# Performance work log

Hardware: AMD Instinct MI355X
Metric: run time of the kernel (lower is better)

Reference implementation:

```python
import jax, jax.numpy as jnp
import numpy as np

B, T, CTX, D, L, H, FF, NMODES = 1024, 512, 23, 320, 5, 8, 1280, 48
DH = D // H
EPS = 1e-5


def layernorm(x, w, b):
    m = jnp.mean(x, axis=-1, keepdims=True)
    v = jnp.mean(jnp.square(x - m), axis=-1, keepdims=True)
    return (x - m) * jax.lax.rsqrt(v + EPS) * w + b


def cheb_sum(x, c):
    """sum_n c[:, n] * T_n(x) via the Chebyshev recurrence, fused with the
    reduction (Clenshaw-style accumulation, no (B,T,N+1) intermediate).
    x: (B,T) in [-1,1], c: (B, N+1)."""
    t_prev = jnp.ones_like(x)           # T_0
    t_cur = x                           # T_1
    acc = c[:, 0:1] * t_prev + c[:, 1:2] * t_cur

    def step(carry, cn):
        tp, tc, a = carry
        tn = 2.0 * x * tc - tp          # T_{n+1}
        return (tc, tn, a + cn[:, None] * tn), None

    (_, _, acc), _ = jax.lax.scan(step, (t_prev, t_cur, acc),
                                  jnp.swapaxes(c[:, 2:], 0, 1))
    return acc


def _forward(k_norm, ctx, W_e, b_e, cls, ln1_w, ln1_b, W_in, b_in, W_out, b_out,
             ln2_w, ln2_b, W1, b1, W2, b2, hln_w, hln_b, Wh1, bh1, Wh2, bh2):
    Bc = ctx.shape[0]
    # elem_proj: Linear(1, D) applied per scalar token -> (B, CTX, D)
    tok = ctx[..., None] * W_e + b_e
    x = jnp.concatenate([jnp.broadcast_to(cls, (Bc, 1, D)), tok], axis=1)  # (B, 24, D)

    def layer(x, p):
        l1w, l1b, win, bin_, wout, bout, l2w, l2b, w1, b1_, w2, b2_ = p
        # --- pre-norm self attention ---
        h = layernorm(x, l1w, l1b)
        qkv = h @ win.T + bin_                      # (B, S, 3D)
        q, k, v = jnp.split(qkv, 3, axis=-1)
        S = x.shape[1]
        q = q.reshape(Bc, S, H, DH)
        k = k.reshape(Bc, S, H, DH)
        v = v.reshape(Bc, S, H, DH)
        scores = jnp.einsum('bqhd,bkhd->bhqk', q, k) / np.sqrt(DH).astype(np.float32)
        a = jax.nn.softmax(scores, axis=-1)
        o = jnp.einsum('bhqk,bkhd->bqhd', a, v).reshape(Bc, S, D)
        x = x + o @ wout.T + bout
        # --- pre-norm FFN ---
        h2 = layernorm(x, l2w, l2b)
        x = x + jax.nn.gelu(h2 @ w1.T + b1_, approximate=False) @ w2.T + b2_
        return x, None

    x, _ = jax.lax.scan(layer, x, (ln1_w, ln1_b, W_in, b_in, W_out, b_out,
                                   ln2_w, ln2_b, W1, b1, W2, b2))
    h = layernorm(x[:, 0], hln_w, hln_b)            # CLS pooling + head LN
    c = jax.nn.gelu(h @ Wh1.T + bh1, approximate=False) @ Wh2.T + bh2  # (B, N+1)
    z = cheb_sum(k_norm, c)
    return jax.nn.sigmoid(z)


def setup_inputs() -> dict:
    key = jax.random.key(0)
    ks = jax.random.split(key, 24)
    rn = lambda k, sh, s=0.02: jax.random.normal(k, sh, jnp.float32) * s
    return {
        'k_norm': jax.random.uniform(ks[0], (B, T), jnp.float32, -1.0, 1.0),
        'ctx': jax.random.normal(ks[1], (B, CTX), jnp.float32),
        'W_e': rn(ks[2], (D,), 0.5),
        'b_e': jnp.zeros((D,), jnp.float32),
        'cls': rn(ks[3], (1, 1, D)),
        'ln1_w': jnp.ones((L, D), jnp.float32),
        'ln1_b': jnp.zeros((L, D), jnp.float32),
        'W_in': rn(ks[4], (L, 3 * D, D)),
        'b_in': jnp.zeros((L, 3 * D), jnp.float32),
        'W_out': rn(ks[5], (L, D, D)),
        'b_out': jnp.zeros((L, D), jnp.float32),
        'ln2_w': jnp.ones((L, D), jnp.float32),
        'ln2_b': jnp.zeros((L, D), jnp.float32),
        'W1': rn(ks[6], (L, FF, D)),
        'b1': jnp.zeros((L, FF), jnp.float32),
        'W2': rn(ks[7], (L, D, FF)),
        'b2': jnp.zeros((L, D), jnp.float32),
        'hln_w': jnp.ones((D,), jnp.float32),
        'hln_b': jnp.zeros((D,), jnp.float32),
        'Wh1': rn(ks[8], (D, D)),
        'bh1': jnp.zeros((D,), jnp.float32),
        'Wh2': rn(ks[9], (NMODES + 1, D)),
        'bh2': jnp.zeros((NMODES + 1,), jnp.float32),
    }


def reference(k_norm, ctx, W_e, b_e, cls, ln1_w, ln1_b, W_in, b_in, W_out, b_out,
              ln2_w, ln2_b, W1, b1, W2, b2, hln_w, hln_b, Wh1, bh1, Wh2, bh2):
    return _forward(k_norm, ctx, W_e, b_e, cls, ln1_w, ln1_b, W_in, b_in, W_out,
                    b_out, ln2_w, ln2_b, W1, b1, W2, b2, hln_w, hln_b, Wh1, bh1,
                    Wh2, bh2)
```

## Files before the change

### kernel.cpp

```cpp
#include <hip/hip_runtime.h>
#include <hip/hip_bf16.h>
#include <math.h>

#define B_SZ 1024
#define T_SZ 512
#define CTX_N 23
#define D 320
#define L_LAYERS 5
#define H 8
#define FF 1280
#define NM1 49
#define S 24
#define DH 40
#define M_ROWS (B_SZ * S)

typedef unsigned short ushort_t;
typedef __attribute__((ext_vector_type(8))) short bfrag8;
typedef __attribute__((ext_vector_type(4))) float facc4;

__device__ __forceinline__ float wave_sum(float v) {
#pragma unroll
  for (int off = 32; off > 0; off >>= 1) v += __shfl_xor(v, off, 64);
  return v;
}

__device__ __forceinline__ float gelu_fast(float x) {
  float t = __builtin_amdgcn_exp2f(x * (2.30211416f + 0.10294404f * x * x));
  return x - x * __builtin_amdgcn_rcpf(t + 1.0f);
}

__device__ __forceinline__ ushort_t f2b(float x) {
  __hip_bfloat16 h = __float2bfloat16(x);
  return *reinterpret_cast<ushort_t*>(&h);
}

__device__ __forceinline__ float b2f(ushort_t u) {
  __hip_bfloat16 h = *reinterpret_cast<__hip_bfloat16*>(&u);
  return __bfloat162float(h);
}

#define GLOAD_LDS16(g, l)                                     \
  __builtin_amdgcn_global_load_lds(                           \
      (const __attribute__((address_space(1))) void*)(g),     \
      (__attribute__((address_space(3))) void*)(l), 16, 0, 0)

__global__ __launch_bounds__(256) void conv_all(
    const float* __restrict__ w_in, const float* __restrict__ w_out,
    const float* __restrict__ w1, const float* __restrict__ w2,
    const float* __restrict__ wh1, ushort_t* __restrict__ dst) {
  int i = blockIdx.x * 256 + threadIdx.x;
  const float* src;
  int off;
  if (i < 384000)       { src = w_in;  off = i; }
  else if (i < 512000)  { src = w_out; off = i - 384000; }
  else if (i < 1024000) { src = w1;    off = i - 512000; }
  else if (i < 1536000) { src = w2;    off = i - 1024000; }
  else                  { src = wh1;   off = i - 1536000; }
  float4 v = ((const float4*)src)[off];
  ushort4 o;
  o.x = f2b(v.x); o.y = f2b(v.y); o.z = f2b(v.z); o.w = f2b(v.w);
  ((ushort4*)dst)[i] = o;
}

__global__ __launch_bounds__(256) void embed_ln(
    const float* __restrict__ ctx, const float* __restrict__ W_e,
    const float* __restrict__ b_e, const float* __restrict__ cls,
    const float* __restrict__ lnw, const float* __restrict__ lnb,
    float* __restrict__ x, ushort_t* __restrict__ y) {
  int wv = threadIdx.x >> 6;
  int lane = threadIdx.x & 63;
  int row = blockIdx.x * 4 + wv;
  int s = row % S;
  int b = row / S;
  float cv = (s == 0) ? 0.f : ctx[b * CTX_N + (s - 1)];
  float v[5];
#pragma unroll
  for (int i = 0; i < 5; i++) {
    int d = lane + 64 * i;
    v[i] = (s == 0) ? cls[d] : cv * W_e[d] + b_e[d];
  }
  float* xr = x + (size_t)row * D;
#pragma unroll
  for (int i = 0; i < 5; i++) xr[lane + 64 * i] = v[i];
  float sm = v[0] + v[1] + v[2] + v[3] + v[4];
  sm = wave_sum(sm);
  float m = sm * (1.0f / (float)D);
  float sq = 0.f;
#pragma unroll
  for (int i = 0; i < 5; i++) { float d0 = v[i] - m; sq += d0 * d0; }
  sq = wave_sum(sq);
  float inv = 1.0f / sqrtf(sq * (1.0f / (float)D) + 1e-5f);
  ushort_t* yr = y + (size_t)row * D;
#pragma unroll
  for (int i = 0; i < 5; i++) {
    int d = lane + 64 * i;
    yr[d] = f2b((v[i] - m) * inv * lnw[d] + lnb[d]);
  }
}

__global__ __launch_bounds__(256) void ln_kernel(
    const float* __restrict__ X, const float* __restrict__ w,
    const float* __restrict__ b, ushort_t* __restrict__ Y,
    int inStride, int outStride) {
  int wv = threadIdx.x >> 6;
  int lane = threadIdx.x & 63;
  int row = blockIdx.x * 4 + wv;
  const float* xr = X + (size_t)row * inStride;
  float v[5];
#pragma unroll
  for (int i = 0; i < 5; i++) v[i] = xr[lane + 64 * i];
  float s = v[0] + v[1] + v[2] + v[3] + v[4];
  s = wave_sum(s);
  float m = s * (1.0f / (float)D);
  float sq = 0.f;
#pragma unroll
  for (int i = 0; i < 5; i++) { float d0 = v[i] - m; sq += d0 * d0; }
  sq = wave_sum(sq);
  float inv = 1.0f / sqrtf(sq * (1.0f / (float)D) + 1e-5f);
  ushort_t* yr = Y + (size_t)row * outStride;
#pragma unroll
  for (int i = 0; i < 5; i++) {
    int d = lane + 64 * i;
    yr[d] = f2b((v[i] - m) * inv * w[d] + b[d]);
  }
}

template <int EPI, int NT, int MT>
__global__ __launch_bounds__(256, 3) void gemm_mfma(
    const ushort_t* __restrict__ A, const ushort_t* __restrict__ W,
    const float* __restrict__ bias, const float* __restrict__ R,
    float* __restrict__ C, ushort_t* __restrict__ Cb,
    const float* __restrict__ lnw, const float* __restrict__ lnb,
    int M, int N, int K) {
  constexpr int BM_ = MT * 32, BK = 64;
  constexpr int BN = 32 * NT;
  constexpr int AR = BM_ / 32;
  constexpr int WR = BN / 32;
  __shared__ __align__(16) ushort_t As[BM_ * BK];
  __shared__ __align__(16) ushort_t Ws[BN * BK];
  __shared__ float psum[2][BM_];
  __shared__ float psq[2][BM_];

  int tid = threadIdx.x;
  int lane = tid & 63;
  int wv = tid >> 6;
  int wvM = wv & 1, wvN = wv >> 1;
  int laneM = lane & 15;
  int kgrp = lane >> 4;
  int sA = laneM & 7;

  int nbx = gridDim.x;
  int lid = blockIdx.x + nbx * blockIdx.y;
  int nchunk = nbx >> 3;
  int mb = (lid & 7) * nchunk + ((lid >> 3) % nchunk);
  int nb = (lid >> 3) / nchunk;
  int m0 = mb * BM_;
  int n0 = nb * BN;

  facc4 acc[MT][NT];
#pragma unroll
  for (int mt = 0; mt < MT; mt++)
#pragma unroll
    for (int nt = 0; nt < NT; nt++) acc[mt][nt] = (facc4){0.f, 0.f, 0.f, 0.f};

  int srow = tid >> 3;
  int jg = (tid & 7) ^ (srow & 7);
  const ushort_t* Ag = A + (size_t)(m0 + srow) * K + jg * 8;
  const ushort_t* Wg = W + (size_t)(n0 + srow) * K + jg * 8;

  for (int k0 = 0; k0 < K; k0 += BK) {
#pragma unroll
    for (int r = 0; r < AR; r++)
      GLOAD_LDS16(Ag + (size_t)r * 32 * K + k0, As + r * 2048 + tid * 8);
#pragma unroll
    for (int r = 0; r < WR; r++)
      GLOAD_LDS16(Wg + (size_t)r * 32 * K + k0, Ws + r * 2048 + tid * 8);
    __syncthreads();
#pragma unroll
    for (int kc = 0; kc < 2; kc++) {
      int jcol = ((kc * 4 + kgrp) ^ sA) * 8;
      bfrag8 af[MT];
#pragma unroll
      for (int mt = 0; mt < MT; mt++) {
        int row = wvM * (MT * 16) + mt * 16 + laneM;
        af[mt] = *(const bfrag8*)&As[row * 64 + jcol];
      }
#pragma unroll
      for (int nt = 0; nt < NT; nt++) {
        int nrow = wvN * (BN / 2) + nt * 16 + laneM;
        bfrag8 bf = *(const bfrag8*)&Ws[nrow * 64 + jcol];
#pragma unroll
        for (int mt = 0; mt < MT; mt++)
          acc[mt][nt] = __builtin_amdgcn_mfma_f32_16x16x32_bf16(
              bf, af[mt], acc[mt][nt], 0, 0, 0);
      }
    }
    __syncthreads();
  }

  if constexpr (EPI == 5) {
    float rs[MT], rq[MT];
#pragma unroll
    for (int mt = 0; mt < MT; mt++) { rs[mt] = 0.f; rq[mt] = 0.f; }
#pragma unroll
    for (int mt = 0; mt < MT; mt++) {
      int m = m0 + wvM * (MT * 16) + mt * 16 + laneM;
#pragma unroll
      for (int nt = 0; nt < NT; nt++) {
        int n = n0 + wvN * (BN / 2) + nt * 16 + kgrp * 4;
        float4 bv = *(const float4*)(bias + n);
        size_t off = (size_t)m * N + n;
        float4 r = *(const float4*)(R + off);
        facc4 a = acc[mt][nt];
        a[0] += bv.x + r.x; a[1] += bv.y + r.y;
        a[2] += bv.z + r.z; a[3] += bv.w + r.w;
        acc[mt][nt] = a;
        rs[mt] += a[0] + a[1] + a[2] + a[3];
        rq[mt] += a[0] * a[0] + a[1] * a[1] + a[2] * a[2] + a[3] * a[3];
      }
    }
#pragma unroll
    for (int mt = 0; mt < MT; mt++) {
      rs[mt] += __shfl_xor(rs[mt], 16, 64);
      rs[mt] += __shfl_xor(rs[mt], 32, 64);
      rq[mt] += __shfl_xor(rq[mt], 16, 64);
      rq[mt] += __shfl_xor(rq[mt], 32, 64);
    }
    if (lane < 16) {
#pragma unroll
      for (int mt = 0; mt < MT; mt++) {
        int lr = wvM * (MT * 16) + mt * 16 + laneM;
        psum[wvN][lr] = rs[mt];
        psq[wvN][lr] = rq[mt];
      }
    }
    __syncthreads();
#pragma unroll
    for (int mt = 0; mt < MT; mt++) {
      int lr = wvM * (MT * 16) + mt * 16 + laneM;
      int m = m0 + lr;
      float ts = psum[0][lr] + psum[1][lr];
      float tq = psq[0][lr] + psq[1][lr];
      float mean = ts * (1.0f / (float)D);
      float var = tq * (1.0f / (float)D) - mean * mean;
      float inv = 1.0f / sqrtf(var + 1e-5f);
#pragma unroll
      for (int nt = 0; nt < NT; nt++) {
        int n = n0 + wvN * (BN / 2) + nt * 16 + kgrp * 4;
        size_t off = (size_t)m * N + n;
        facc4 a = acc[mt][nt];
        *(float4*)(C + off) = (float4){a[0], a[1], a[2], a[3]};
        float4 w4 = *(const float4*)(lnw + n);
        float4 b4 = *(const float4*)(lnb + n);
        ushort4 o;
        o.x = f2b((a[0] - mean) * inv * w4.x + b4.x);
        o.y = f2b((a[1] - mean) * inv * w4.y + b4.y);
        o.z = f2b((a[2] - mean) * inv * w4.z + b4.z);
        o.w = f2b((a[3] - mean) * inv * w4.w + b4.w);
        *(ushort4*)(Cb + off) = o;
      }
    }
  } else {
#pragma unroll
    for (int mt = 0; mt < MT; mt++) {
      int m = m0 + wvM * (MT * 16) + mt * 16 + laneM;
#pragma unroll
      for (int nt = 0; nt < NT; nt++) {
        int n = n0 + wvN * (BN / 2) + nt * 16 + kgrp * 4;
        float4 bv = *(const float4*)(bias + n);
        facc4 a = acc[mt][nt];
        float v0 = a[0] + bv.x, v1 = a[1] + bv.y, v2 = a[2] + bv.z,
              v3 = a[3] + bv.w;
        size_t off = (size_t)m * N + n;
        if constexpr (EPI == 1) {
          ushort4 o;
          o.x = f2b(gelu_fast(v0)); o.y = f2b(gelu_fast(v1));
          o.z = f2b(gelu_fast(v2)); o.w = f2b(gelu_fast(v3));
          *(ushort4*)(Cb + off) = o;
        } else if constexpr (EPI == 2) {
          float4 r = *(const float4*)(R + off);
          float4 o = {v0 + r.x, v1 + r.y, v2 + r.z, v3 + r.w};
          *(float4*)(C + off) = o;
        } else if constexpr (EPI == 3) {
          float4 o = {gelu_fast(v0), gelu_fast(v1), gelu_fast(v2),
                      gelu_fast(v3)};
          *(float4*)(C + off) = o;
        } else {
          ushort4 o;
          o.x = f2b(v0); o.y = f2b(v1); o.z = f2b(v2); o.w = f2b(v3);
          *(ushort4*)(Cb + off) = o;
        }
      }
    }
  }
}

__global__ __launch_bounds__(256) void attn_kernel(
    const ushort_t* __restrict__ qkv, ushort_t* __restrict__ o) {
  int b = blockIdx.x >> 3;
  int h = blockIdx.x & 7;
  __shared__ __align__(16) float q[S][44];
  __shared__ __align__(16) float v[S][44];
  __shared__ __align__(16) float kT[DH][28];
  __shared__ __align__(16) float sc[S][28];
  int tid = threadIdx.x;
  const ushort_t* base = qkv + (size_t)b * S * (3 * D) + h * DH;

  for (int idx = tid; idx < 720; idx += 256) {
    int t = idx / 240;
    int r = idx % 240;
    int s = r / 10, dg = r % 10;
    ushort4 u = *(const ushort4*)(base + (size_t)s * (3 * D) + t * D + dg * 4);
    float4 f = {b2f(u.x), b2f(u.y), b2f(u.z), b2f(u.w)};
    if (t == 0) {
      *(float4*)&q[s][dg * 4] = f;
    } else if (t == 2) {
      *(float4*)&v[s][dg * 4] = f;
    } else {
      kT[dg * 4 + 0][s] = f.x;
      kT[dg * 4 + 1][s] = f.y;
      kT[dg * 4 + 2][s] = f.z;
      kT[dg * 4 + 3][s] = f.w;
    }
  }
  __syncthreads();

  if (tid < 144) {
    int i = tid / 6, jg = tid % 6;
    facc4 acc = {0.f, 0.f, 0.f, 0.f};
#pragma unroll
    for (int d = 0; d < DH; d++) {
      float qv = q[i][d];
      float4 kv = *(const float4*)&kT[d][jg * 4];
      acc[0] += qv * kv.x; acc[1] += qv * kv.y;
      acc[2] += qv * kv.z; acc[3] += qv * kv.w;
    }
    const float sca = 0.15811388300841897f;
    float4 ov = {acc[0] * sca, acc[1] * sca, acc[2] * sca, acc[3] * sca};
    *(float4*)&sc[i][jg * 4] = ov;
  }
  __syncthreads();

  if (tid < S) {
    float mx = -1e30f;
#pragma unroll
    for (int j = 0; j < S; j++) mx = fmaxf(mx, sc[tid][j]);
    float sum = 0.f;
#pragma unroll
    for (int j = 0; j < S; j++) {
      float e = __expf(sc[tid][j] - mx);
      sc[tid][j] = e;
      sum += e;
    }
    float rr = 1.0f / sum;
#pragma unroll
    for (int j = 0; j < S; j++) sc[tid][j] *= rr;
  }
  __syncthreads();

  if (tid < 240) {
    int i = tid / 10, dg = tid % 10;
    facc4 acc = {0.f, 0.f, 0.f, 0.f};
#pragma unroll
    for (int j = 0; j < S; j++) {
      float p = sc[i][j];
      float4 vv = *(const float4*)&v[j][dg * 4];
      acc[0] += p * vv.x; acc[1] += p * vv.y;
      acc[2] += p * vv.z; acc[3] += p * vv.w;
    }
    ushort4 ov;
    ov.x = f2b(acc[0]); ov.y = f2b(acc[1]);
    ov.z = f2b(acc[2]); ov.w = f2b(acc[3]);
    *(ushort4*)(o + (size_t)b * S * D + (size_t)i * D + h * DH + dg * 4) = ov;
  }
}

__global__ __launch_bounds__(256) void head_cheb(
    const float* __restrict__ g, const float* __restrict__ Wh2,
    const float* __restrict__ bh2, const float* __restrict__ k_norm,
    float* __restrict__ out) {
  int b = blockIdx.x;
  __shared__ float gs[D];
  __shared__ float cs[NM1];
  int tid = threadIdx.x;
  for (int i = tid; i < D; i += 256) gs[i] = g[(size_t)b * D + i];
  __syncthreads();
  if (tid < NM1) {
    const float* wr = Wh2 + (size_t)tid * D;
    float s = bh2[tid];
    for (int d = 0; d < D; d++) s += gs[d] * wr[d];
    cs[tid] = s;
  }
  __syncthreads();
  for (int t = tid; t < T_SZ; t += 256) {
    float xv = k_norm[(size_t)b * T_SZ + t];
    float tp = 1.f, tc = xv;
    float acc = cs[0] + cs[1] * xv;
#pragma unroll
    for (int n = 2; n < NM1; n++) {
      float tn = 2.f * xv * tc - tp;
      acc += cs[n] * tn;
      tp = tc;
      tc = tn;
    }
    out[(size_t)b * T_SZ + t] = 1.f / (1.f + expf(-acc));
  }
}

extern "C" void kernel_launch(void* const* d_in, const int* in_sizes, int n_in,
                              void* d_out, int out_size, void* d_ws,
                              size_t ws_size, hipStream_t stream) {
  const float* k_norm = (const float*)d_in[0];
  const float* ctx    = (const float*)d_in[1];
  const float* W_e    = (const float*)d_in[2];
  const float* b_e    = (const float*)d_in[3];
  const float* cls    = (const float*)d_in[4];
  const float* ln1_w  = (const float*)d_in[5];
  const float* ln1_b  = (const float*)d_in[6];
  const float* W_in   = (const float*)d_in[7];
  const float* b_in   = (const float*)d_in[8];
  const float* W_out  = (const float*)d_in[9];
  const float* b_out  = (const float*)d_in[10];
  const float* ln2_w  = (const float*)d_in[11];
  const float* ln2_b  = (const float*)d_in[12];
  const float* W1     = (const float*)d_in[13];
  const float* b1     = (const float*)d_in[14];
  const float* W2     = (const float*)d_in[15];
  const float* b2     = (const float*)d_in[16];
  const float* hln_w  = (const float*)d_in[17];
  const float* hln_b  = (const float*)d_in[18];
  const float* Wh1    = (const float*)d_in[19];
  const float* bh1    = (const float*)d_in[20];
  const float* Wh2    = (const float*)d_in[21];
  const float* bh2    = (const float*)d_in[22];
  float* out = (float*)d_out;

  float* x = (float*)d_ws;
  ushort_t* hbuf = (ushort_t*)(x + (size_t)M_ROWS * D);
  ushort_t* big = hbuf + (size_t)M_ROWS * D;
  ushort_t* wb_in = big + (size_t)M_ROWS * FF;
  ushort_t* wb_out = wb_in + (size_t)L_LAYERS * 3 * D * D;
  ushort_t* wb1 = wb_out + (size_t)L_LAYERS * D * D;
  ushort_t* wb2 = wb1 + (size_t)L_LAYERS * FF * D;
  ushort_t* wbh1 = wb2 + (size_t)L_LAYERS * D * FF;
  ushort_t* hcls = wbh1 + (size_t)D * D;
  float* ghead = (float*)(hcls + (size_t)B_SZ * D);
  ushort_t* abuf = big + (size_t)M_ROWS * 960;

  conv_all<<<6100, 256, 0, stream>>>(W_in, W_out, W1, W2, Wh1, wb_in);

  embed_ln<<<M_ROWS / 4, 256, 0, stream>>>(ctx, W_e, b_e, cls, ln1_w, ln1_b,
                                           x, hbuf);

  for (int l = 0; l < L_LAYERS; l++) {
    gemm_mfma<4, 5, 4><<<dim3(M_ROWS / 128, (3 * D) / 160), 256, 0, stream>>>(
        hbuf, wb_in + (size_t)l * 3 * D * D, b_in + (size_t)l * 3 * D, nullptr,
        nullptr, big, nullptr, nullptr, M_ROWS, 3 * D, D);
    attn_kernel<<<B_SZ * H, 256, 0, stream>>>(big, abuf);
    gemm_mfma<5, 10, 2><<<dim3(M_ROWS / 64, 1), 256, 0, stream>>>(
        abuf, wb_out + (size_t)l * D * D, b_out + (size_t)l * D, x, x, hbuf,
        ln2_w + (size_t)l * D, ln2_b + (size_t)l * D, M_ROWS, D, D);
    gemm_mfma<1, 5, 4><<<dim3(M_ROWS / 128, FF / 160), 256, 0, stream>>>(
        hbuf, wb1 + (size_t)l * FF * D, b1 + (size_t)l * FF, nullptr, nullptr,
        big, nullptr, nullptr, M_ROWS, FF, D);
    if (l + 1 < L_LAYERS) {
      gemm_mfma<5, 10, 2><<<dim3(M_ROWS / 64, 1), 256, 0, stream>>>(
          big, wb2 + (size_t)l * D * FF, b2 + (size_t)l * D, x, x, hbuf,
          ln1_w + (size_t)(l + 1) * D, ln1_b + (size_t)(l + 1) * D,
          M_ROWS, D, FF);
    } else {
      gemm_mfma<2, 5, 2><<<dim3(M_ROWS / 64, D / 160), 256, 0, stream>>>(
          big, wb2 + (size_t)l * D * FF, b2 + (size_t)l * D, x, x, nullptr,
          nullptr, nullptr, M_ROWS, D, FF);
    }
  }

  ln_kernel<<<B_SZ / 4, 256, 0, stream>>>(x, hln_w, hln_b, hcls, S * D, D);
  gemm_mfma<3, 5, 2><<<dim3(B_SZ / 64, D / 160), 256, 0, stream>>>(
      hcls, wbh1, bh1, nullptr, ghead, nullptr, nullptr, nullptr, B_SZ, D, D);
  head_cheb<<<B_SZ, 256, 0, stream>>>(ghead, Wh2, bh2, k_norm, out);
}
```

Measured before the change: 994.5 us.

## Compute only CLS rows after last-layer attention

```diff
diff --git a/kernel.cpp b/kernel.cpp
--- a/kernel.cpp
+++ b/kernel.cpp
@@ -131,15 +131,15 @@
     const float* __restrict__ bias, const float* __restrict__ R,
     float* __restrict__ C, ushort_t* __restrict__ Cb,
     const float* __restrict__ lnw, const float* __restrict__ lnb,
-    int M, int N, int K) {
+    int M, int N, int K, int gath) {
   constexpr int BM_ = MT * 32, BK = 64;
   constexpr int BN = 32 * NT;
   constexpr int AR = BM_ / 32;
   constexpr int WR = BN / 32;
   __shared__ __align__(16) ushort_t As[BM_ * BK];
   __shared__ __align__(16) ushort_t Ws[BN * BK];
-  __shared__ float psum[2][BM_];
-  __shared__ float psq[2][BM_];
+  __shared__ float psum[2][(EPI == 5) ? BM_ : 4];
+  __shared__ float psq[2][(EPI == 5) ? BM_ : 4];
 
   int tid = threadIdx.x;
   int lane = tid & 63;
@@ -165,13 +165,13 @@
 
   int srow = tid >> 3;
   int jg = (tid & 7) ^ (srow & 7);
-  const ushort_t* Ag = A + (size_t)(m0 + srow) * K + jg * 8;
+  const ushort_t* Ag = A + (size_t)(m0 + srow) * gath * K + jg * 8;
   const ushort_t* Wg = W + (size_t)(n0 + srow) * K + jg * 8;
 
   for (int k0 = 0; k0 < K; k0 += BK) {
 #pragma unroll
     for (int r = 0; r < AR; r++)
-      GLOAD_LDS16(Ag + (size_t)r * 32 * K + k0, As + r * 2048 + tid * 8);
+      GLOAD_LDS16(Ag + (size_t)r * 32 * gath * K + k0, As + r * 2048 + tid * 8);
 #pragma unroll
     for (int r = 0; r < WR; r++)
       GLOAD_LDS16(Wg + (size_t)r * 32 * K + k0, Ws + r * 2048 + tid * 8);
@@ -209,8 +209,8 @@
       for (int nt = 0; nt < NT; nt++) {
         int n = n0 + wvN * (BN / 2) + nt * 16 + kgrp * 4;
         float4 bv = *(const float4*)(bias + n);
-        size_t off = (size_t)m * N + n;
-        float4 r = *(const float4*)(R + off);
+        size_t offR = (size_t)m * gath * N + n;
+        float4 r = *(const float4*)(R + offR);
         facc4 a = acc[mt][nt];
         a[0] += bv.x + r.x; a[1] += bv.y + r.y;
         a[2] += bv.z + r.z; a[3] += bv.w + r.w;
@@ -445,6 +445,9 @@
   ushort_t* wbh1 = wb2 + (size_t)L_LAYERS * D * FF;
   ushort_t* hcls = wbh1 + (size_t)D * D;
   float* ghead = (float*)(hcls + (size_t)B_SZ * D);
+  float* xc = ghead + (size_t)B_SZ * D;
+  ushort_t* hbufc = (ushort_t*)(xc + (size_t)B_SZ * D);
+  ushort_t* bigc = hbufc + (size_t)B_SZ * D;
   ushort_t* abuf = big + (size_t)M_ROWS * 960;
 
   conv_all<<<6100, 256, 0, stream>>>(W_in, W_out, W1, W2, Wh1, wb_in);
@@ -455,28 +458,36 @@
   for (int l = 0; l < L_LAYERS; l++) {
     gemm_mfma<4, 5, 4><<<dim3(M_ROWS / 128, (3 * D) / 160), 256, 0, stream>>>(
         hbuf, wb_in + (size_t)l * 3 * D * D, b_in + (size_t)l * 3 * D, nullptr,
-        nullptr, big, nullptr, nullptr, M_ROWS, 3 * D, D);
+        nullptr, big, nullptr, nullptr, M_ROWS, 3 * D, D, 1);
     attn_kernel<<<B_SZ * H, 256, 0, stream>>>(big, abuf);
-    gemm_mfma<5, 10, 2><<<dim3(M_ROWS / 64, 1), 256, 0, stream>>>(
-        abuf, wb_out + (size_t)l * D * D, b_out + (size_t)l * D, x, x, hbuf,
-        ln2_w + (size_t)l * D, ln2_b + (size_t)l * D, M_ROWS, D, D);
-    gemm_mfma<1, 5, 4><<<dim3(M_ROWS / 128, FF / 160), 256, 0, stream>>>(
-        hbuf, wb1 + (size_t)l * FF * D, b1 + (size_t)l * FF, nullptr, nullptr,
-        big, nullptr, nullptr, M_ROWS, FF, D);
     if (l + 1 < L_LAYERS) {
+      gemm_mfma<5, 10, 2><<<dim3(M_ROWS / 64, 1), 256, 0, stream>>>(
+          abuf, wb_out + (size_t)l * D * D, b_out + (size_t)l * D, x, x, hbuf,
+          ln2_w + (size_t)l * D, ln2_b + (size_t)l * D, M_ROWS, D, D, 1);
+      gemm_mfma<1, 5, 4><<<dim3(M_ROWS / 128, FF / 160), 256, 0, stream>>>(
+          hbuf, wb1 + (size_t)l * FF * D, b1 + (size_t)l * FF, nullptr,
+          nullptr, big, nullptr, nullptr, M_ROWS, FF, D, 1);
       gemm_mfma<5, 10, 2><<<dim3(M_ROWS / 64, 1), 256, 0, stream>>>(
           big, wb2 + (size_t)l * D * FF, b2 + (size_t)l * D, x, x, hbuf,
           ln1_w + (size_t)(l + 1) * D, ln1_b + (size_t)(l + 1) * D,
-          M_ROWS, D, FF);
+          M_ROWS, D, FF, 1);
     } else {
-      gemm_mfma<2, 5, 2><<<dim3(M_ROWS / 64, D / 160), 256, 0, stream>>>(
-          big, wb2 + (size_t)l * D * FF, b2 + (size_t)l * D, x, x, nullptr,
-          nullptr, nullptr, M_ROWS, D, FF);
-    }
-  }
-
-  ln_kernel<<<B_SZ / 4, 256, 0, stream>>>(x, hln_w, hln_b, hcls, S * D, D);
+      gemm_mfma<5, 10, 2><<<dim3(B_SZ / 64, 1), 256, 0, stream>>>(
+          abuf, wb_out + (size_t)l * D * D, b_out + (size_t)l * D, x, xc,
+          hbufc, ln2_w + (size_t)l * D, ln2_b + (size_t)l * D,
+          B_SZ, D, D, S);
+      gemm_mfma<1, 5, 4><<<dim3(B_SZ / 128, FF / 160), 256, 0, stream>>>(
+          hbufc, wb1 + (size_t)l * FF * D, b1 + (size_t)l * FF, nullptr,
+          nullptr, bigc, nullptr, nullptr, B_SZ, FF, D, 1);
+      gemm_mfma<2, 5, 2><<<dim3(B_SZ / 64, D / 160), 256, 0, stream>>>(
+          bigc, wb2 + (size_t)l * D * FF, b2 + (size_t)l * D, xc, xc, nullptr,
+          nullptr, nullptr, B_SZ, D, FF, 1);
+    }
+  }
+
+  ln_kernel<<<B_SZ / 4, 256, 0, stream>>>(xc, hln_w, hln_b, hcls, D, D);
   gemm_mfma<3, 5, 2><<<dim3(B_SZ / 64, D / 160), 256, 0, stream>>>(
-      hcls, wbh1, bh1, nullptr, ghead, nullptr, nullptr, nullptr, B_SZ, D, D);
+      hcls, wbh1, bh1, nullptr, ghead, nullptr, nullptr, nullptr,
+      B_SZ, D, D, 1);
   head_cheb<<<B_SZ, 256, 0, stream>>>(ghead, Wh2, bh2, k_norm, out);
 }
```

New measurement: 953.8 us, median of 2. 4.1% less time.
